# Kernel optimization log

Measured on AMD Instinct MI355X. Metric: run time of the kernel, lower is better.

Reference implementation:

```python
import jax, jax.numpy as jnp
import numpy as np

# 4th-order symplectic (Forest-Ruth / Yoshida) coefficients
_C13 = 2.0 ** (1.0 / 3.0)
_DEN = 2.0 - _C13
C_COEF = (0.5 / _DEN, (0.5 - 2.0 ** (-2.0 / 3.0)) / _DEN,
          (0.5 - 2.0 ** (-2.0 / 3.0)) / _DEN, 0.5 / _DEN)
D_COEF = (1.0 / _DEN, -_C13 / _DEN, 1.0 / _DEN, 0.0)
EPS = 0.01  # tol passed to NeuralODE


def setup_inputs() -> dict:
    key = jax.random.key(0)
    k1, k2 = jax.random.split(key)
    B, N = 4, 1048576  # batch of trajectories x particles (elementwise state)
    return {
        "p0": jax.random.normal(k1, (B, N), dtype=jnp.float32),
        "q0": jax.random.normal(k2, (B, N), dtype=jnp.float32),
        "t0": jnp.zeros((), dtype=jnp.float32),
        "t1": jnp.ones((), dtype=jnp.float32),
    }


def _integrate(p0, q0, t0, t1, n_steps):
    h = (t1 - t0) / n_steps

    def step(carry, _):
        kp, kq = carry
        # 4 symplectic substeps, unrolled (coefficients are compile-time consts)
        for c, d in zip(C_COEF, D_COEF):
            tq = kq + c * kp * h            # Tp(p) = p
            kp = kp - d * jnp.sin(tq) * h   # Vq(q) = sin(q)
            kq = tq
        return (kp, kq), None

    (kp, kq), _ = jax.lax.scan(step, (p0, q0), None, length=n_steps)
    return kp, kq


def reference(p0, q0, t0, t1):
    # n_steps = round(max|t1-t0| / (4*eps)); concrete (non-traced) like the .item() in torch
    n_steps = int(np.round(float(jnp.abs(t1 - t0).max()) / (EPS * 4)))
    return _integrate(p0, q0, t0, t1, n_steps)
```

## Files before the change

### kernel.cpp

```cpp
#include <hip/hip_runtime.h>


#define NSTEPS 25

typedef float v2f __attribute__((ext_vector_type(2)));

__device__ __forceinline__ v2f pk_fma(v2f a, v2f b, v2f c) {
    v2f d;
    asm("v_pk_fma_f32 %0, %1, %2, %3" : "=v"(d) : "v"(a), "v"(b), "v"(c));
    return d;
}

__global__ __launch_bounds__(256) void symp4_kernel(
    const float4* __restrict__ p0,
    const float4* __restrict__ q0,
    const float* __restrict__ t0,
    const float* __restrict__ t1,
    float4* __restrict__ out_p,
    float4* __restrict__ out_q,
    int nthreads)
{
    const int tid = blockIdx.x * blockDim.x + threadIdx.x;
    if (tid >= nthreads) return;

    const float h = (t1[0] - t0[0]) * (1.0f / (float)NSTEPS);

    const float INV2PI = 0.15915494309189535f;
    const float TWOPI  = 6.283185307179586f;

    const float c1hr = 0.10752506536265768f  * h;
    const float c2hr = -0.02794866718106242f * h;
    const float nd1h = -1.3512071919596578f  * h;
    const float nd2h =  1.7024143839193153f  * h;

    const v2f c1v = {c1hr, c1hr};
    const v2f c2v = {c2hr, c2hr};
    const v2f d1v = {nd1h, nd1h};
    const v2f d2v = {nd2h, nd2h};

    float4 pa = p0[2 * tid], pb = p0[2 * tid + 1];
    float4 qa = q0[2 * tid], qb = q0[2 * tid + 1];

    v2f P[4] = {{pa.x, pa.y}, {pa.z, pa.w}, {pb.x, pb.y}, {pb.z, pb.w}};
    v2f Q[4] = {{qa.x * INV2PI, qa.y * INV2PI}, {qa.z * INV2PI, qa.w * INV2PI},
                {qb.x * INV2PI, qb.y * INV2PI}, {qb.z * INV2PI, qb.w * INV2PI}};

    for (int s = 0; s < NSTEPS; ++s) {
        #pragma unroll
        for (int j = 0; j < 4; ++j) Q[j] = pk_fma(c1v, P[j], Q[j]);
        #pragma unroll
        for (int j = 0; j < 4; ++j) {
            v2f sv;
            sv.x = __builtin_amdgcn_sinf(Q[j].x);
            sv.y = __builtin_amdgcn_sinf(Q[j].y);
            P[j] = pk_fma(d1v, sv, P[j]);
        }
        #pragma unroll
        for (int j = 0; j < 4; ++j) Q[j] = pk_fma(c2v, P[j], Q[j]);
        #pragma unroll
        for (int j = 0; j < 4; ++j) {
            v2f sv;
            sv.x = __builtin_amdgcn_sinf(Q[j].x);
            sv.y = __builtin_amdgcn_sinf(Q[j].y);
            P[j] = pk_fma(d2v, sv, P[j]);
        }
        #pragma unroll
        for (int j = 0; j < 4; ++j) Q[j] = pk_fma(c2v, P[j], Q[j]);
        #pragma unroll
        for (int j = 0; j < 4; ++j) {
            v2f sv;
            sv.x = __builtin_amdgcn_sinf(Q[j].x);
            sv.y = __builtin_amdgcn_sinf(Q[j].y);
            P[j] = pk_fma(d1v, sv, P[j]);
        }
        #pragma unroll
        for (int j = 0; j < 4; ++j) Q[j] = pk_fma(c1v, P[j], Q[j]);
    }

    out_p[2 * tid]     = make_float4(P[0].x, P[0].y, P[1].x, P[1].y);
    out_p[2 * tid + 1] = make_float4(P[2].x, P[2].y, P[3].x, P[3].y);
    out_q[2 * tid]     = make_float4(Q[0].x * TWOPI, Q[0].y * TWOPI,
                                     Q[1].x * TWOPI, Q[1].y * TWOPI);
    out_q[2 * tid + 1] = make_float4(Q[2].x * TWOPI, Q[2].y * TWOPI,
                                     Q[3].x * TWOPI, Q[3].y * TWOPI);
}

extern "C" void kernel_launch(void* const* d_in, const int* in_sizes, int n_in,
                              void* d_out, int out_size, void* d_ws, size_t ws_size,
                              hipStream_t stream) {
    const float* p0 = (const float*)d_in[0];
    const float* q0 = (const float*)d_in[1];
    const float* t0 = (const float*)d_in[2];
    const float* t1 = (const float*)d_in[3];
    float* out = (float*)d_out;

    const int n = in_sizes[0];
    const int nthreads = n / 8;
    const int block = 256;
    const int grid = (nthreads + block - 1) / block;

    symp4_kernel<<<grid, block, 0, stream>>>(
        (const float4*)p0, (const float4*)q0, t0, t1,
        (float4*)out, (float4*)(out + n), nthreads);
}
```

Baseline: 107.7 us.

## Split sine evaluation between transcendental unit and polynomial on VALU, merge drift steps

Half of each thread's eight elements keep using the hardware sin instruction. The other half use range reduction with rintf plus a degree-7 odd polynomial with the step coefficient folded in. Integer turn counts are accumulated so the output position can be rebuilt at the end. The goal is to spread work across the transcendental and FMA pipes so the quarter-rate sin unit is no longer the bottleneck. The adjacent c1 drift substeps across iterations are merged into one 2*c1 FMA with a correction after the loop, and packed FMAs are replaced by scalar fmaf. This adds accuracy risk from the polynomial approximation and from the changed coefficient rounding.

Result: slower. 119.8 us (+11.2%).

```diff
diff --git a/kernel.cpp b/kernel.cpp
--- a/kernel.cpp
+++ b/kernel.cpp
@@ -2,14 +2,6 @@
 
 
 #define NSTEPS 25
-
-typedef float v2f __attribute__((ext_vector_type(2)));
-
-__device__ __forceinline__ v2f pk_fma(v2f a, v2f b, v2f c) {
-    v2f d;
-    asm("v_pk_fma_f32 %0, %1, %2, %3" : "=v"(d) : "v"(a), "v"(b), "v"(c));
-    return d;
-}
 
 __global__ __launch_bounds__(256) void symp4_kernel(
     const float4* __restrict__ p0,
@@ -28,61 +20,94 @@
     const float INV2PI = 0.15915494309189535f;
     const float TWOPI  = 6.283185307179586f;
 
-    const float c1hr = 0.10752506536265768f  * h;
-    const float c2hr = -0.02794866718106242f * h;
-    const float nd1h = -1.3512071919596578f  * h;
-    const float nd2h =  1.7024143839193153f  * h;
+    const float c1hr  =  0.10752506536265768f * h;
+    const float c2hr  = -0.02794866718106242f * h;
+    const float tc1hr =  0.21505013072531536f * h;
+    const float nd1h  = -1.3512071919596578f * h;
+    const float nd2h  =  1.7024143839193155f * h;
 
-    const v2f c1v = {c1hr, c1hr};
-    const v2f c2v = {c2hr, c2hr};
-    const v2f d1v = {nd1h, nd1h};
-    const v2f d2v = {nd2h, nd2h};
+    const float C1 =  6.2786440f;
+    const float C3 = -41.0925120f;
+    const float C5 =  77.9162880f;
+    const float C7 = -56.0496640f;
+    const float K11 = C1 * nd1h, K13 = C3 * nd1h, K15 = C5 * nd1h, K17 = C7 * nd1h;
+    const float K21 = C1 * nd2h, K23 = C3 * nd2h, K25 = C5 * nd2h, K27 = C7 * nd2h;
 
     float4 pa = p0[2 * tid], pb = p0[2 * tid + 1];
     float4 qa = q0[2 * tid], qb = q0[2 * tid + 1];
 
-    v2f P[4] = {{pa.x, pa.y}, {pa.z, pa.w}, {pb.x, pb.y}, {pb.z, pb.w}};
-    v2f Q[4] = {{qa.x * INV2PI, qa.y * INV2PI}, {qa.z * INV2PI, qa.w * INV2PI},
-                {qb.x * INV2PI, qb.y * INV2PI}, {qb.z * INV2PI, qb.w * INV2PI}};
+    float P[8] = {pa.x, pa.y, pa.z, pa.w, pb.x, pb.y, pb.z, pb.w};
+    float Q[8] = {qa.x * INV2PI, qa.y * INV2PI, qa.z * INV2PI, qa.w * INV2PI,
+                  qb.x * INV2PI, qb.y * INV2PI, qb.z * INV2PI, qb.w * INV2PI};
+    float N[4] = {0.f, 0.f, 0.f, 0.f};
 
+    #pragma unroll
+    for (int j = 0; j < 8; ++j) Q[j] = fmaf(c1hr, P[j], Q[j]);
+
+    #pragma unroll 1
     for (int s = 0; s < NSTEPS; ++s) {
         #pragma unroll
-        for (int j = 0; j < 4; ++j) Q[j] = pk_fma(c1v, P[j], Q[j]);
+        for (int j = 4; j < 8; ++j) {
+            float n = rintf(Q[j]);
+            N[j - 4] += n;
+            Q[j] -= n;
+        }
+
         #pragma unroll
-        for (int j = 0; j < 4; ++j) {
-            v2f sv;
-            sv.x = __builtin_amdgcn_sinf(Q[j].x);
-            sv.y = __builtin_amdgcn_sinf(Q[j].y);
-            P[j] = pk_fma(d1v, sv, P[j]);
+        for (int j = 0; j < 4; ++j)
+            P[j] = fmaf(nd1h, __builtin_amdgcn_sinf(Q[j]), P[j]);
+        #pragma unroll
+        for (int j = 4; j < 8; ++j) {
+            float u = Q[j] * Q[j];
+            float H = fmaf(K17, u, K15);
+            H = fmaf(H, u, K13);
+            H = fmaf(H, u, K11);
+            P[j] = fmaf(Q[j], H, P[j]);
         }
         #pragma unroll
-        for (int j = 0; j < 4; ++j) Q[j] = pk_fma(c2v, P[j], Q[j]);
+        for (int j = 0; j < 8; ++j) Q[j] = fmaf(c2hr, P[j], Q[j]);
+
         #pragma unroll
-        for (int j = 0; j < 4; ++j) {
-            v2f sv;
-            sv.x = __builtin_amdgcn_sinf(Q[j].x);
-            sv.y = __builtin_amdgcn_sinf(Q[j].y);
-            P[j] = pk_fma(d2v, sv, P[j]);
+        for (int j = 0; j < 4; ++j)
+            P[j] = fmaf(nd2h, __builtin_amdgcn_sinf(Q[j]), P[j]);
+        #pragma unroll
+        for (int j = 4; j < 8; ++j) {
+            float u = Q[j] * Q[j];
+            float H = fmaf(K27, u, K25);
+            H = fmaf(H, u, K23);
+            H = fmaf(H, u, K21);
+            P[j] = fmaf(Q[j], H, P[j]);
         }
         #pragma unroll
-        for (int j = 0; j < 4; ++j) Q[j] = pk_fma(c2v, P[j], Q[j]);
+        for (int j = 0; j < 8; ++j) Q[j] = fmaf(c2hr, P[j], Q[j]);
+
         #pragma unroll
-        for (int j = 0; j < 4; ++j) {
-            v2f sv;
-            sv.x = __builtin_amdgcn_sinf(Q[j].x);
-            sv.y = __builtin_amdgcn_sinf(Q[j].y);
-            P[j] = pk_fma(d1v, sv, P[j]);
+        for (int j = 0; j < 4; ++j)
+            P[j] = fmaf(nd1h, __builtin_amdgcn_sinf(Q[j]), P[j]);
+        #pragma unroll
+        for (int j = 4; j < 8; ++j) {
+            float u = Q[j] * Q[j];
+            float H = fmaf(K17, u, K15);
+            H = fmaf(H, u, K13);
+            H = fmaf(H, u, K11);
+            P[j] = fmaf(Q[j], H, P[j]);
         }
         #pragma unroll
-        for (int j = 0; j < 4; ++j) Q[j] = pk_fma(c1v, P[j], Q[j]);
+        for (int j = 0; j < 8; ++j) Q[j] = fmaf(tc1hr, P[j], Q[j]);
     }
 
-    out_p[2 * tid]     = make_float4(P[0].x, P[0].y, P[1].x, P[1].y);
-    out_p[2 * tid + 1] = make_float4(P[2].x, P[2].y, P[3].x, P[3].y);
-    out_q[2 * tid]     = make_float4(Q[0].x * TWOPI, Q[0].y * TWOPI,
-                                     Q[1].x * TWOPI, Q[1].y * TWOPI);
-    out_q[2 * tid + 1] = make_float4(Q[2].x * TWOPI, Q[2].y * TWOPI,
-                                     Q[3].x * TWOPI, Q[3].y * TWOPI);
+    float QO[8];
+    #pragma unroll
+    for (int j = 0; j < 8; ++j) {
+        float t = fmaf(-c1hr, P[j], Q[j]);
+        if (j >= 4) t += N[j - 4];
+        QO[j] = t * TWOPI;
+    }
+
+    out_p[2 * tid]     = make_float4(P[0], P[1], P[2], P[3]);
+    out_p[2 * tid + 1] = make_float4(P[4], P[5], P[6], P[7]);
+    out_q[2 * tid]     = make_float4(QO[0], QO[1], QO[2], QO[3]);
+    out_q[2 * tid + 1] = make_float4(QO[4], QO[5], QO[6], QO[7]);
 }
 
 extern "C" void kernel_launch(void* const* d_in, const int* in_sizes, int n_in,
```
